# Optimization experiments

Hardware: AMD Instinct MI355X
Metric: run time of the kernel (lower is better)

## Reference

```python
import jax, jax.numpy as jnp
import numpy as np

B, S, D = 2, 2048, 1024
H, HD, K = 16, 64, 4
F = 4096
EPS = 1e-6
ROPE_BASE = 10000.0
NEG = -1e9


def rmsnorm(x, w):
    return x * jax.lax.rsqrt(jnp.mean(x * x, axis=-1, keepdims=True) + EPS) * w


def rope(t, pos):
    # t: (B,S,H,HD), pos: (B,S,H) per-node position (float)
    inv_freq = 1.0 / (ROPE_BASE ** (jnp.arange(0, HD, 2, dtype=jnp.float32) / HD))
    ang = pos[..., None] * inv_freq  # (B,S,H,HD/2)
    cos, sin = jnp.cos(ang), jnp.sin(ang)
    t1, t2 = t[..., : HD // 2], t[..., HD // 2:]
    return jnp.concatenate([t1 * cos - t2 * sin, t2 * cos + t1 * sin], axis=-1)


def setup_inputs() -> dict:
    key = jax.random.key(0)
    ks = jax.random.split(key, 12)
    s = lambda d: 1.0 / np.sqrt(d)
    return {
        "x": jax.random.normal(ks[0], (B, S, D), jnp.float32),
        "attn_norm_w": jnp.ones((D,), jnp.float32),
        "ffn_norm_w": jnp.ones((D,), jnp.float32),
        "Wq": jax.random.normal(ks[1], (D, H * HD), jnp.float32) * s(D),
        "Wk": jax.random.normal(ks[2], (D, H * HD), jnp.float32) * s(D),
        "Wv": jax.random.normal(ks[3], (D, H * HD), jnp.float32) * s(D),
        "Wo": jax.random.normal(ks[4], (H * HD, D), jnp.float32) * s(H * HD),
        "Wr": jax.random.normal(ks[5], (D, H * K), jnp.float32) * s(D),
        "w1": jax.random.normal(ks[6], (D, F), jnp.float32) * s(D),
        "w2": jax.random.normal(ks[7], (D, F), jnp.float32) * s(D),
        "w3": jax.random.normal(ks[8], (F, D), jnp.float32) * s(F),
    }


def reference(x, attn_norm_w, ffn_norm_w, Wq, Wk, Wv, Wo, Wr, w1, w2, w3):
    # ---- pre-norm + hypergraph node-routed causal attention ----
    h = rmsnorm(x, attn_norm_w)
    # per-(token, head) routing to K hyper-nodes
    logits = (h @ Wr).reshape(B, S, H, K)
    node = jnp.argmax(logits, axis=-1)                      # (B,S,H) int
    onehot = jax.nn.one_hot(node, K, dtype=jnp.float32)     # (B,S,H,K)
    # per-node RoPE position: count of previous same-node tokens
    cum = jnp.cumsum(onehot, axis=1)                        # inclusive
    pos = jnp.take_along_axis(cum, node[..., None], axis=-1)[..., 0] - 1.0  # (B,S,H)

    q = (h @ Wq).reshape(B, S, H, HD)
    k = (h @ Wk).reshape(B, S, H, HD)
    v = (h @ Wv).reshape(B, S, H, HD)
    q = rope(q, pos)
    k = rope(k, pos)

    scores = jnp.einsum("bqhd,bkhd->bhqk", q, k) / np.sqrt(HD)  # (B,H,S,S)
    node_h = jnp.transpose(node, (0, 2, 1))                     # (B,H,S)
    same = node_h[:, :, :, None] == node_h[:, :, None, :]       # intra-node only
    causal = jnp.tril(jnp.ones((S, S), bool))
    allowed = same & causal
    attn = jax.nn.softmax(jnp.where(allowed, scores, NEG), axis=-1)
    ctx = jnp.einsum("bhqk,bkhd->bqhd", attn, v).reshape(B, S, H * HD)
    x = x + ctx @ Wo

    # ---- pre-norm + SwiGLU ----
    h2 = rmsnorm(x, ffn_norm_w)
    ffn = (jax.nn.silu(h2 @ w1) * (h2 @ w2)) @ w3
    return x + ffn
```

## Files before the change

### kernel.cpp

```cpp
#include <hip/hip_runtime.h>
#include <hip/hip_bf16.h>
#include <math.h>

typedef __hip_bfloat16 bf16;

#define B_  2
#define S_  2048
#define D_  1024
#define H_  16
#define HD_ 64
#define KR_ 4
#define F_  4096
#define TOK (B_*S_)
#define NEG (-1.0e9f)

typedef __attribute__((ext_vector_type(8))) short bf16x8_t;
typedef __attribute__((ext_vector_type(4))) float f32x4_t;
typedef unsigned int u32;
#define AS1 __attribute__((address_space(1)))
#define AS3 __attribute__((address_space(3)))

__device__ __forceinline__ float u2f(unsigned short u) {
  union { float f; unsigned int i; } cv; cv.i = ((unsigned int)u) << 16; return cv.f;
}
__device__ __forceinline__ unsigned short f2u(float f) {
  return (unsigned short)(__bfloat16_as_ushort(__float2bfloat16(f)));
}

__device__ __forceinline__ void gl_lds16(const bf16* g, unsigned short* lds_base) {
  __builtin_amdgcn_global_load_lds((const AS1 u32*)g, (AS3 u32*)lds_base, 16, 0, 0);
}

__device__ __forceinline__ float rd1(const void* p, size_t i, bool isbf) {
  return isbf ? __bfloat162float(((const bf16*)p)[i]) : ((const float*)p)[i];
}

__device__ __forceinline__ void xcd_tile(int& bx, int& by) {
  const int nx = gridDim.x;
  const int nwg = nx * gridDim.y;
  const int hw = blockIdx.y * nx + blockIdx.x;
  const int tile = (hw & 7) * (nwg >> 3) + (hw >> 3);
  bx = tile % nx;
  by = tile / nx;
}

#define SWZ_SK8(lane)   (((((lane) & 3) ^ (((lane) >> 3) & 3))) << 3)
#define SWZ_RK(colv)    ((((colv) >> 1) & 3))

__global__ __launch_bounds__(256) void prep_k(
    const void* Wq, const void* Wk, const void* Wv, const void* Wo,
    const void* w1, const void* w2, const void* w3,
    bf16* __restrict__ qkvT, bf16* __restrict__ WoT,
    bf16* __restrict__ w1T, bf16* __restrict__ w2T, bf16* __restrict__ w3T,
    const void* Wr, float* __restrict__ Wrf,
    const unsigned* __restrict__ anw_words, int* __restrict__ flag) {
  const bool isbf = (anw_words[0] == 0x3F803F80u);
  const int bid = blockIdx.x;
  const int tid = threadIdx.x;
  if (bid == 0 && tid == 0) *flag = isbf ? 1 : 0;
  if (bid >= 16384) {
    const int i = (bid - 16384) * 256 + tid;
    Wrf[i] = rd1(Wr, i, isbf);
    return;
  }
  const void* W; bf16* WT; int K, N, nx, local;
  if (bid < 4096) {
    const int wi = bid >> 10; local = bid & 1023; K = 1024; N = 1024; nx = 32;
    W = (wi == 0) ? Wq : (wi == 1) ? Wk : (wi == 2) ? Wv : Wo;
    WT = (wi == 3) ? WoT : qkvT + ((size_t)wi << 20);
  } else if (bid < 8192)  { W = w1; WT = w1T; local = bid - 4096;  K = 1024; N = 4096; nx = 128; }
  else if (bid < 12288)   { W = w2; WT = w2T; local = bid - 8192;  K = 1024; N = 4096; nx = 128; }
  else                    { W = w3; WT = w3T; local = bid - 12288; K = 4096; N = 1024; nx = 32; }
  __shared__ float tile[32][33];
  const int n0 = (local % nx) * 32, k0 = (local / nx) * 32;
  const int rl = tid >> 5, cl = tid & 31;
#pragma unroll
  for (int i = 0; i < 4; i++)
    tile[rl + 8 * i][cl] = rd1(W, (size_t)(k0 + rl + 8 * i) * N + n0 + cl, isbf);
  __syncthreads();
#pragma unroll
  for (int i = 0; i < 4; i++)
    WT[(size_t)(n0 + rl + 8 * i) * K + k0 + cl] = __float2bfloat16(tile[cl][rl + 8 * i]);
}

template <bool XDUAL, bool WF>
__global__ __launch_bounds__(256) void rmsnorm_k(const void* x, const void* w,
                                                 bf16* __restrict__ ob,
                                                 float* __restrict__ of,
                                                 const int* __restrict__ flagp) {
  const bool isbf = (*flagp != 0);
  const int row = blockIdx.x;
  const int t = threadIdx.x;
  float v[4];
  float ss = 0.f;
#pragma unroll
  for (int i = 0; i < 4; i++) {
    const size_t idx = (size_t)row * D_ + t + 256 * i;
    v[i] = XDUAL ? rd1(x, idx, isbf) : ((const float*)x)[idx];
    ss += v[i] * v[i];
  }
#pragma unroll
  for (int off = 32; off >= 1; off >>= 1) ss += __shfl_down(ss, off);
  __shared__ float red[4];
  if ((t & 63) == 0) red[t >> 6] = ss;
  __syncthreads();
  const float tot = red[0] + red[1] + red[2] + red[3];
  const float sc = rsqrtf(tot * (1.f / D_) + 1e-6f);
#pragma unroll
  for (int i = 0; i < 4; i++) {
    const int c = t + 256 * i;
    const float r = v[i] * sc * rd1(w, c, isbf);
    ob[(size_t)row * D_ + c] = __float2bfloat16(r);
    if (WF) of[(size_t)row * D_ + c] = r;
  }
}

__global__ __launch_bounds__(256) void router_k(const float* __restrict__ h,
                                                const float* __restrict__ Wrf,
                                                int* __restrict__ node) {
  const int tok0 = blockIdx.x * 16;
  const int t = threadIdx.x;
  __shared__ float hs[16][1024];
  __shared__ float lg[16][64];
  {
    const float4* hsrc = (const float4*)(h + (size_t)tok0 * D_);
    float4* hdst = (float4*)hs;
#pragma unroll
    for (int j = 0; j < 16; j++) hdst[j * 256 + t] = hsrc[j * 256 + t];
  }
  __syncthreads();
  const int col = t & 63, tg = t >> 6;
  float acc[4] = {0.f, 0.f, 0.f, 0.f};
  for (int i = 0; i < D_; i += 4) {
    float wv[4];
#pragma unroll
    for (int u = 0; u < 4; u++) wv[u] = Wrf[(size_t)(i + u) * 64 + col];
#pragma unroll
    for (int tt = 0; tt < 4; tt++) {
      const float4 hv = *(const float4*)&hs[tg * 4 + tt][i];
      acc[tt] = fmaf(hv.x, wv[0], acc[tt]);
      acc[tt] = fmaf(hv.y, wv[1], acc[tt]);
      acc[tt] = fmaf(hv.z, wv[2], acc[tt]);
      acc[tt] = fmaf(hv.w, wv[3], acc[tt]);
    }
  }
#pragma unroll
  for (int tt = 0; tt < 4; tt++) lg[tg * 4 + tt][col] = acc[tt];
  __syncthreads();
  const int tok = t >> 4, hh = t & 15;
  const float* l = &lg[tok][hh * 4];
  float best = l[0];
  int bi = 0;
#pragma unroll
  for (int j = 1; j < KR_; j++) {
    const float vv = l[j];
    if (vv > best) { best = vv; bi = j; }
  }
  node[(size_t)(tok0 + tok) * H_ + hh] = bi;
}

__global__ __launch_bounds__(256) void pos_k(const int* __restrict__ node,
                                             float* __restrict__ pos,
                                             unsigned short* __restrict__ iperm,
                                             unsigned char* __restrict__ gid,
                                             int* __restrict__ gstart) {
  const int bh = blockIdx.x;
  const int b = bh >> 4, h = bh & 15;
  const int t = threadIdx.x;
  __shared__ int sc[256][4];
  int vals[8];
  int c[4] = {0, 0, 0, 0};
#pragma unroll
  for (int i = 0; i < 8; i++) {
    vals[i] = node[(size_t)(b * S_ + t * 8 + i) * H_ + h] & 3;
    c[vals[i]]++;
  }
#pragma unroll
  for (int n = 0; n < 4; n++) sc[t][n] = c[n];
  __syncthreads();
  for (int off = 1; off < 256; off <<= 1) {
    int add[4] = {0, 0, 0, 0};
    if (t >= off) {
#pragma unroll
      for (int n = 0; n < 4; n++) add[n] = sc[t - off][n];
    }
    __syncthreads();
#pragma unroll
    for (int n = 0; n < 4; n++) sc[t][n] += add[n];
    __syncthreads();
  }
  int start[4];
#pragma unroll
  for (int n = 0; n < 4; n++) start[n] = sc[t][n] - c[n];
  int gs[4];
  gs[0] = 0;
  gs[1] = sc[255][0];
  gs[2] = gs[1] + sc[255][1];
  gs[3] = gs[2] + sc[255][2];
  if (t < 4) gstart[bh * 4 + t] = gs[t];
  const size_t bhS = (size_t)bh * S_;
#pragma unroll
  for (int i = 0; i < 8; i++) {
    const int n = vals[i];
    const int rank = start[n]++;
    pos[(size_t)(b * S_ + t * 8 + i) * H_ + h] = (float)rank;
    const int newp = gs[n] + rank;
    iperm[bhS + newp] = (unsigned short)(t * 8 + i);
    gid[bhS + newp] = (unsigned char)n;
  }
}

__global__ __launch_bounds__(256) void attn_k(const bf16* __restrict__ q,
                                              const bf16* __restrict__ k,
                                              const bf16* __restrict__ v,
                                              const unsigned short* __restrict__ ip,
                                              const unsigned char* __restrict__ gidp,
                                              const int* __restrict__ gstart,
                                              bf16* __restrict__ ctx) {
  const int qt = 31 - blockIdx.x;
  const int h = blockIdx.y;
  const int b = blockIdx.z;
  const int bS = b * S_;
  const int bh = b * H_ + h;
  const size_t bhS = (size_t)bh * S_;
  const int tid = threadIdx.x;
  const int w = tid >> 6;
  const int lane = tid & 63;
  const int col = lane & 15;
  const int quad = lane >> 4;

  __shared__ unsigned short Qs[64][76];
  __shared__ unsigned short Ks[64][76];
  __shared__ unsigned short Vst[64][76];
  __shared__ unsigned short Pa[64][76];

  {
    const int qr = tid & 63, ds = (tid >> 6) * 16;
    const int ipq = ip[bhS + qt * 64 + qr];
    const bf16* src = q + (size_t)(bS + ipq) * D_ + h * HD_ + ds;
#pragma unroll
    for (int i = 0; i < 4; i++)
      *(ushort4*)&Qs[qr][ds + 4 * i] = *(const ushort4*)(src + 4 * i);
  }
  int gq_r[4];
#pragma unroll
  for (int reg = 0; reg < 4; reg++)
    gq_r[reg] = gidp[bhS + qt * 64 + w * 16 + quad * 4 + reg];
  float m_r[4] = {NEG, NEG, NEG, NEG};
  float l_r[4] = {0.f, 0.f, 0.f, 0.f};

  f32x4_t acc_o[4];
#pragma unroll
  for (int ct = 0; ct < 4; ct++) acc_o[ct] = (f32x4_t){0.f, 0.f, 0.f, 0.f};

  const int kt0 = gstart[bh * 4 + gidp[bhS + qt * 64]] >> 6;

  for (int kt = kt0; kt <= qt; kt++) {
    __syncthreads();
    {
      const int key = tid & 63, ds = (tid >> 6) * 16;
      const int ipk = ip[bhS + kt * 64 + key];
      const bf16* ksrc = k + (size_t)(bS + ipk) * D_ + h * HD_ + ds;
      const bf16* vsrc = v + (size_t)(bS + ipk) * D_ + h * HD_ + ds;
#pragma unroll
      for (int i = 0; i < 4; i++) {
        *(ushort4*)&Ks[key][ds + 4 * i] = *(const ushort4*)(ksrc + 4 * i);
        const ushort4 vu = *(const ushort4*)(vsrc + 4 * i);
        Vst[ds + 4 * i + 0][key] = vu.x;
        Vst[ds + 4 * i + 1][key] = vu.y;
        Vst[ds + 4 * i + 2][key] = vu.z;
        Vst[ds + 4 * i + 3][key] = vu.w;
      }
    }
    __syncthreads();

    f32x4_t s[4];
    {
      const bf16x8_t a0 = *(const bf16x8_t*)&Qs[w * 16 + col][quad * 8];
      const bf16x8_t a1 = *(const bf16x8_t*)&Qs[w * 16 + col][32 + quad * 8];
#pragma unroll
      for (int ct = 0; ct < 4; ct++) {
        f32x4_t acc = (f32x4_t){0.f, 0.f, 0.f, 0.f};
        const bf16x8_t b0 = *(const bf16x8_t*)&Ks[ct * 16 + col][quad * 8];
        const bf16x8_t b1 = *(const bf16x8_t*)&Ks[ct * 16 + col][32 + quad * 8];
        acc = __builtin_amdgcn_mfma_f32_16x16x32_bf16(a0, b0, acc, 0, 0, 0);
        acc = __builtin_amdgcn_mfma_f32_16x16x32_bf16(a1, b1, acc, 0, 0, 0);
        s[ct] = acc;
      }
    }
    const bool diag = (kt == qt);
    const size_t kbase = bhS + kt * 64;
    const int gk[4] = {gidp[kbase + col], gidp[kbase + 16 + col],
                       gidp[kbase + 32 + col], gidp[kbase + 48 + col]};
#pragma unroll
    for (int ct = 0; ct < 4; ct++) {
#pragma unroll
      for (int reg = 0; reg < 4; reg++) {
        const int qr = quad * 4 + reg;
        const int kc = ct * 16 + col;
        const bool ok = (gk[ct] == gq_r[reg]) && (!diag || kc <= w * 16 + qr);
        s[ct][reg] = ok ? (s[ct][reg] * 0.125f) : NEG;
      }
    }
    float al[4];
#pragma unroll
    for (int reg = 0; reg < 4; reg++) {
      float tm = fmaxf(fmaxf(s[0][reg], s[1][reg]), fmaxf(s[2][reg], s[3][reg]));
#pragma unroll
      for (int off = 1; off <= 8; off <<= 1) tm = fmaxf(tm, __shfl_xor(tm, off));
      const float mold = m_r[reg];
      const float mnew = fmaxf(mold, tm);
      const bool dead = (mnew <= -5.0e8f);
      const float alpha = dead ? 1.f : __expf(mold - mnew);
      float rowsum = 0.f;
      const int qr = w * 16 + quad * 4 + reg;
#pragma unroll
      for (int ct = 0; ct < 4; ct++) {
        const float e = dead ? 0.f : __expf(s[ct][reg] - mnew);
        rowsum += e;
        Pa[qr][ct * 16 + col] = f2u(e);
      }
#pragma unroll
      for (int off = 1; off <= 8; off <<= 1) rowsum += __shfl_xor(rowsum, off);
      l_r[reg] = l_r[reg] * alpha + rowsum;
      m_r[reg] = mnew;
      al[reg] = alpha;
    }
    {
      const bf16x8_t pa0 = *(const bf16x8_t*)&Pa[w * 16 + col][quad * 8];
      const bf16x8_t pa1 = *(const bf16x8_t*)&Pa[w * 16 + col][32 + quad * 8];
#pragma unroll
      for (int ct = 0; ct < 4; ct++) {
#pragma unroll
        for (int reg = 0; reg < 4; reg++) acc_o[ct][reg] *= al[reg];
        const bf16x8_t b0 = *(const bf16x8_t*)&Vst[ct * 16 + col][quad * 8];
        const bf16x8_t b1 = *(const bf16x8_t*)&Vst[ct * 16 + col][32 + quad * 8];
        acc_o[ct] = __builtin_amdgcn_mfma_f32_16x16x32_bf16(pa0, b0, acc_o[ct], 0, 0, 0);
        acc_o[ct] = __builtin_amdgcn_mfma_f32_16x16x32_bf16(pa1, b1, acc_o[ct], 0, 0, 0);
      }
    }
  }

#pragma unroll
  for (int reg = 0; reg < 4; reg++) {
    const int qr = w * 16 + quad * 4 + reg;
    const int op = ip[bhS + qt * 64 + qr];
    const float l = l_r[reg];
    const float invl = (l > 0.f) ? (1.f / l) : 0.f;
#pragma unroll
    for (int ct = 0; ct < 4; ct++) {
      ctx[(size_t)(bS + op) * D_ + h * HD_ + ct * 16 + col] =
          __float2bfloat16(acc_o[ct][reg] * invl);
    }
  }
}

template <int EPI>
__global__ __launch_bounds__(256) void mgemm_k(const bf16* __restrict__ A,
                                               const bf16* __restrict__ BT,
                                               float* __restrict__ Cf,
                                               void* Cout,
                                               const void* resdual,
                                               const float* __restrict__ resf,
                                               const float* __restrict__ posp,
                                               const int* __restrict__ flagp,
                                               int N, int Kd) {
  const bool isbf = (*flagp != 0);
  __shared__ unsigned short As[2][128][32];
  __shared__ unsigned short Bs[2][128][32];
  const int tid = threadIdx.x;
  const int w = tid >> 6, lane = tid & 63;
  const int col = lane & 15, quad = lane >> 4;
  const int wm = w & 1, wn = w >> 1;
  int bx, by;
  xcd_tile(bx, by);
  const int row0 = by * 128, col0 = bx * 128;

  const int srow = lane >> 2, sk8 = SWZ_SK8(lane);
  const bf16* Ag0 = A + (size_t)(row0 + 16 * w + srow) * Kd + sk8;
  const bf16* Ag1 = A + (size_t)(row0 + 64 + 16 * w + srow) * Kd + sk8;
  const bf16* Bg0 = BT + (size_t)(col0 + 16 * w + srow) * Kd + sk8;
  const bf16* Bg1 = BT + (size_t)(col0 + 64 + 16 * w + srow) * Kd + sk8;
  const int rk = SWZ_RK(col);

  f32x4_t acc[4][4];
#pragma unroll
  for (int i = 0; i < 4; i++)
#pragma unroll
    for (int j = 0; j < 4; j++) acc[i][j] = (f32x4_t){0.f, 0.f, 0.f, 0.f};

  gl_lds16(Ag0, &As[0][16 * w][0]);
  gl_lds16(Ag1, &As[0][64 + 16 * w][0]);
  gl_lds16(Bg0, &Bs[0][16 * w][0]);
  gl_lds16(Bg1, &Bs[0][64 + 16 * w][0]);
  __syncthreads();

  int cur = 0;
  for (int kt = 0; kt < Kd; kt += 32) {
    const int nxt = cur ^ 1;
    if (kt + 32 < Kd) {
      gl_lds16(Ag0 + kt + 32, &As[nxt][16 * w][0]);
      gl_lds16(Ag1 + kt + 32, &As[nxt][64 + 16 * w][0]);
      gl_lds16(Bg0 + kt + 32, &Bs[nxt][16 * w][0]);
      gl_lds16(Bg1 + kt + 32, &Bs[nxt][64 + 16 * w][0]);
    }
    bf16x8_t af[4], bfr[4];
#pragma unroll
    for (int i = 0; i < 4; i++) {
      af[i] = *(const bf16x8_t*)&As[cur][wm * 64 + i * 16 + col][(quad ^ rk) * 8];
      bfr[i] = *(const bf16x8_t*)&Bs[cur][wn * 64 + i * 16 + col][(quad ^ rk) * 8];
    }
#pragma unroll
    for (int i = 0; i < 4; i++)
#pragma unroll
      for (int j = 0; j < 4; j++)
        acc[i][j] = __builtin_amdgcn_mfma_f32_16x16x32_bf16(af[i], bfr[j], acc[i][j], 0, 0, 0);
    __syncthreads();
    cur = nxt;
  }

  if (EPI == 0) {
    const int ng_base = col0 + wn * 64;
    const int sec = ng_base >> 10;
    bf16* outp = (bf16*)Cout + (size_t)sec * ((size_t)TOK * D_);
    if (sec < 2) {
      const int hh = (ng_base & 1023) >> 6;
      const float c0 = 13.287712379549449f / 32.f;
      const float inv0 = exp2f(-(float)col * c0);
      const float inv1 = exp2f(-(float)(col + 16) * c0);
#pragma unroll
      for (int i = 0; i < 4; i++) {
#pragma unroll
        for (int reg = 0; reg < 4; reg++) {
          const int m = row0 + wm * 64 + i * 16 + quad * 4 + reg;
          const float p = posp[m * H_ + hh];
          float sn0, cs0, sn1, cs1;
          sincosf(p * inv0, &sn0, &cs0);
          sincosf(p * inv1, &sn1, &cs1);
          const float a0 = acc[i][0][reg], b0 = acc[i][2][reg];
          const float a1 = acc[i][1][reg], b1 = acc[i][3][reg];
          bf16* rowp = outp + (size_t)m * D_ + hh * 64;
          rowp[col]      = __float2bfloat16(a0 * cs0 - b0 * sn0);
          rowp[col + 32] = __float2bfloat16(b0 * cs0 + a0 * sn0);
          rowp[col + 16] = __float2bfloat16(a1 * cs1 - b1 * sn1);
          rowp[col + 48] = __float2bfloat16(b1 * cs1 + a1 * sn1);
        }
      }
    } else {
#pragma unroll
      for (int i = 0; i < 4; i++)
#pragma unroll
        for (int j = 0; j < 4; j++)
#pragma unroll
          for (int reg = 0; reg < 4; reg++) {
            const int m = row0 + wm * 64 + i * 16 + quad * 4 + reg;
            const int ng = col0 + wn * 64 + j * 16 + col;
            outp[(size_t)m * D_ + (ng & 1023)] = __float2bfloat16(acc[i][j][reg]);
          }
    }
  } else {
#pragma unroll
    for (int i = 0; i < 4; i++) {
#pragma unroll
      for (int j = 0; j < 4; j++) {
#pragma unroll
        for (int reg = 0; reg < 4; reg++) {
          const int m = row0 + wm * 64 + i * 16 + quad * 4 + reg;
          const int nl = wn * 64 + j * 16 + col;
          const size_t idx = (size_t)m * N + col0 + nl;
          if (EPI == 1) {
            Cf[idx] = acc[i][j][reg] + rd1(resdual, idx, isbf);
          } else {
            const float r = acc[i][j][reg] + resf[idx];
            if (isbf) ((bf16*)Cout)[idx] = __float2bfloat16(r);
            else      ((float*)Cout)[idx] = r;
          }
        }
      }
    }
  }
}

template <int EPI>
__global__ __launch_bounds__(256) void mgemm64_k(const bf16* __restrict__ A,
                                                 const bf16* __restrict__ BT,
                                                 float* __restrict__ Cf,
                                                 void* Cout,
                                                 const void* resdual,
                                                 const float* __restrict__ resf,
                                                 const int* __restrict__ flagp,
                                                 int N, int Kd) {
  const bool isbf = (*flagp != 0);
  __shared__ unsigned short As[2][2][64][32];
  __shared__ unsigned short Bs[2][2][128][32];
  const int tid = threadIdx.x;
  const int w = tid >> 6, lane = tid & 63;
  const int col = lane & 15, quad = lane >> 4;
  int bx, by;
  xcd_tile(bx, by);
  const int row0 = by * 64, col0 = bx * 128;

  const int srow = lane >> 2, sk8 = SWZ_SK8(lane);
  const bf16* Ag  = A + (size_t)(row0 + 16 * w + srow) * Kd + sk8;
  const bf16* Bg0 = BT + (size_t)(col0 + 32 * w + srow) * Kd + sk8;
  const bf16* Bg1 = BT + (size_t)(col0 + 32 * w + 16 + srow) * Kd + sk8;
  const int rk = SWZ_RK(col);

  f32x4_t acc[4][2];
#pragma unroll
  for (int i = 0; i < 4; i++)
#pragma unroll
    for (int j = 0; j < 2; j++) acc[i][j] = (f32x4_t){0.f, 0.f, 0.f, 0.f};

  auto stage = [&](int buf, int kt) {
#pragma unroll
    for (int hh = 0; hh < 2; hh++) {
      gl_lds16(Ag + kt + 32 * hh, &As[buf][hh][16 * w][0]);
      gl_lds16(Bg0 + kt + 32 * hh, &Bs[buf][hh][32 * w][0]);
      gl_lds16(Bg1 + kt + 32 * hh, &Bs[buf][hh][32 * w + 16][0]);
    }
  };

  stage(0, 0);
  __syncthreads();

  int cur = 0;
  for (int kt = 0; kt < Kd; kt += 64) {
    const int nxt = cur ^ 1;
    if (kt + 64 < Kd) stage(nxt, kt + 64);
#pragma unroll
    for (int hh = 0; hh < 2; hh++) {
      bf16x8_t af[4], bfr[2];
#pragma unroll
      for (int i = 0; i < 4; i++)
        af[i] = *(const bf16x8_t*)&As[cur][hh][i * 16 + col][(quad ^ rk) * 8];
#pragma unroll
      for (int j = 0; j < 2; j++)
        bfr[j] = *(const bf16x8_t*)&Bs[cur][hh][w * 32 + j * 16 + col][(quad ^ rk) * 8];
#pragma unroll
      for (int i = 0; i < 4; i++)
#pragma unroll
        for (int j = 0; j < 2; j++)
          acc[i][j] = __builtin_amdgcn_mfma_f32_16x16x32_bf16(af[i], bfr[j], acc[i][j], 0, 0, 0);
    }
    __syncthreads();
    cur = nxt;
  }

#pragma unroll
  for (int i = 0; i < 4; i++) {
#pragma unroll
    for (int j = 0; j < 2; j++) {
#pragma unroll
      for (int reg = 0; reg < 4; reg++) {
        const int m = row0 + i * 16 + quad * 4 + reg;
        const int nl = w * 32 + j * 16 + col;
        const size_t idx = (size_t)m * N + col0 + nl;
        if (EPI == 1) {
          Cf[idx] = acc[i][j][reg] + rd1(resdual, idx, isbf);
        } else {
          const float r = acc[i][j][reg] + resf[idx];
          if (isbf) ((bf16*)Cout)[idx] = __float2bfloat16(r);
          else      ((float*)Cout)[idx] = r;
        }
      }
    }
  }
}

__global__ __launch_bounds__(256) void mgate_k(const bf16* __restrict__ A,
                                               const bf16* __restrict__ B1T,
                                               const bf16* __restrict__ B2T,
                                               bf16* __restrict__ G,
                                               int Kd) {
  __shared__ unsigned short As[2][128][32];
  __shared__ unsigned short Bs1[2][64][32];
  __shared__ unsigned short Bs2[2][64][32];
  const int tid = threadIdx.x;
  const int w = tid >> 6, lane = tid & 63;
  const int col = lane & 15, quad = lane >> 4;
  const int wm = w & 1, wn = w >> 1;
  const int hw = blockIdx.y * gridDim.x + blockIdx.x;
  const int rect = hw & 7, inner = hw >> 3;
  const int by = ((rect >> 2) << 4) | (inner >> 4);
  const int bx = ((rect & 3) << 4) | (inner & 15);
  const int row0 = by * 128, col0 = bx * 64;

  const int srow = lane >> 2, sk8 = SWZ_SK8(lane);
  const bf16* Ag0 = A + (size_t)(row0 + 16 * w + srow) * Kd + sk8;
  const bf16* Ag1 = A + (size_t)(row0 + 64 + 16 * w + srow) * Kd + sk8;
  const bf16* B1g = B1T + (size_t)(col0 + 16 * w + srow) * Kd + sk8;
  const bf16* B2g = B2T + (size_t)(col0 + 16 * w + srow) * Kd + sk8;
  const int rk = SWZ_RK(col);

  f32x4_t acc1[4][2], acc2[4][2];
#pragma unroll
  for (int i = 0; i < 4; i++)
#pragma unroll
    for (int j = 0; j < 2; j++) {
      acc1[i][j] = (f32x4_t){0.f, 0.f, 0.f, 0.f};
      acc2[i][j] = (f32x4_t){0.f, 0.f, 0.f, 0.f};
    }

  gl_lds16(Ag0, &As[0][16 * w][0]);
  gl_lds16(Ag1, &As[0][64 + 16 * w][0]);
  gl_lds16(B1g, &Bs1[0][16 * w][0]);
  gl_lds16(B2g, &Bs2[0][16 * w][0]);
  __syncthreads();

  int cur = 0;
  for (int kt = 0; kt < Kd; kt += 32) {
    const int nxt = cur ^ 1;
    if (kt + 32 < Kd) {
      gl_lds16(Ag0 + kt + 32, &As[nxt][16 * w][0]);
      gl_lds16(Ag1 + kt + 32, &As[nxt][64 + 16 * w][0]);
      gl_lds16(B1g + kt + 32, &Bs1[nxt][16 * w][0]);
      gl_lds16(B2g + kt + 32, &Bs2[nxt][16 * w][0]);
    }
    bf16x8_t af[4], b1f[2], b2f[2];
#pragma unroll
    for (int i = 0; i < 4; i++)
      af[i] = *(const bf16x8_t*)&As[cur][wm * 64 + i * 16 + col][(quad ^ rk) * 8];
#pragma unroll
    for (int j = 0; j < 2; j++) {
      b1f[j] = *(const bf16x8_t*)&Bs1[cur][wn * 32 + j * 16 + col][(quad ^ rk) * 8];
      b2f[j] = *(const bf16x8_t*)&Bs2[cur][wn * 32 + j * 16 + col][(quad ^ rk) * 8];
    }
#pragma unroll
    for (int i = 0; i < 4; i++)
#pragma unroll
      for (int j = 0; j < 2; j++) {
        acc1[i][j] = __builtin_amdgcn_mfma_f32_16x16x32_bf16(af[i], b1f[j], acc1[i][j], 0, 0, 0);
        acc2[i][j] = __builtin_amdgcn_mfma_f32_16x16x32_bf16(af[i], b2f[j], acc2[i][j], 0, 0, 0);
      }
    __syncthreads();
    cur = nxt;
  }

#pragma unroll
  for (int i = 0; i < 4; i++) {
#pragma unroll
    for (int j = 0; j < 2; j++) {
#pragma unroll
      for (int reg = 0; reg < 4; reg++) {
        const int m = row0 + wm * 64 + i * 16 + quad * 4 + reg;
        const int n = col0 + wn * 32 + j * 16 + col;
        const float z = acc1[i][j][reg];
        const float sig = 1.f / (1.f + __expf(-z));
        G[(size_t)m * F_ + n] = __float2bfloat16(z * sig * acc2[i][j][reg]);
      }
    }
  }
}

extern "C" void kernel_launch(void* const* d_in, const int* in_sizes, int n_in,
                              void* d_out, int out_size, void* d_ws, size_t ws_size,
                              hipStream_t stream) {
  const void* x   = d_in[0];
  const void* anw = d_in[1];
  const void* fnw = d_in[2];
  const void* Wq  = d_in[3];
  const void* Wk  = d_in[4];
  const void* Wv  = d_in[5];
  const void* Wo  = d_in[6];
  const void* Wr  = d_in[7];
  const void* w1  = d_in[8];
  const void* w2  = d_in[9];
  const void* w3  = d_in[10];

  char* ws = (char*)d_ws;
  int*   node = (int*)ws;
  float* pos  = (float*)(ws + (256 << 10));
  int*   flag = (int*)(ws + (512 << 10));
  unsigned short* iperm = (unsigned short*)(ws + (640u << 10));
  unsigned char*  gidb  = (unsigned char*)(ws + (768u << 10));
  int*   gstart = (int*)(ws + (832u << 10));
  float* x2   = (float*)(ws + (1u << 20));
  bf16*  ctx  = (bf16*)(ws + (17u << 20));
  bf16*  h2   = ctx;
  float* Wrf  = (float*)(ws + (17u << 20));
  char*  r0   = ws + (25u << 20);
  bf16*  hb   = (bf16*)(r0);
  bf16*  qb   = (bf16*)(r0 + (8u << 20));
  bf16*  kb   = (bf16*)(r0 + (16u << 20));
  bf16*  vb   = (bf16*)(r0 + (24u << 20));
  float* hf   = (float*)(r0 + (8u << 20));
  bf16*  g    = (bf16*)(r0);
  bf16*  qkvT = (bf16*)(ws + (57u << 20));
  bf16*  WoT  = (bf16*)(ws + (63u << 20));
  bf16*  w1T  = (bf16*)(ws + (65u << 20));
  bf16*  w2T  = (bf16*)(ws + (73u << 20));
  bf16*  w3T  = (bf16*)(ws + (81u << 20));

  prep_k<<<16640, 256, 0, stream>>>(Wq, Wk, Wv, Wo, w1, w2, w3,
                                    qkvT, WoT, w1T, w2T, w3T,
                                    Wr, Wrf, (const unsigned*)anw, flag);
  rmsnorm_k<true, true><<<TOK, 256, 0, stream>>>(x, anw, hb, hf, flag);
  router_k<<<TOK / 16, 256, 0, stream>>>(hf, Wrf, node);
  pos_k<<<32, 256, 0, stream>>>(node, pos, iperm, gidb, gstart);
  mgemm_k<0><<<dim3(3072 / 128, TOK / 128), 256, 0, stream>>>(hb, qkvT, nullptr, qb, nullptr, nullptr, pos, flag, 3072, D_);
  attn_k<<<dim3(S_ / 64, H_, B_), 256, 0, stream>>>(qb, kb, vb, iperm, gidb, gstart, ctx);
  mgemm64_k<1><<<dim3(D_ / 128, TOK / 64), 256, 0, stream>>>(ctx, WoT, x2, nullptr, x, nullptr, flag, D_, D_);
  rmsnorm_k<false, false><<<TOK, 256, 0, stream>>>(x2, fnw, h2, nullptr, flag);
  mgate_k<<<dim3(F_ / 64, TOK / 128), 256, 0, stream>>>(h2, w1T, w2T, g, D_);
  mgemm64_k<2><<<dim3(D_ / 128, TOK / 64), 256, 0, stream>>>(g, w3T, nullptr, d_out, nullptr, x2, flag, D_, F_);
}
```

Baseline: 465.1 us.

## Triple-buffer LDS in GEMM kernels with partial vmcnt waits

Converts the three MFMA GEMM kernels from double-buffered to triple-buffered LDS staging with a prefetch distance of two k-tiles. __syncthreads is replaced by an explicit s_waitcnt vmcnt(n) plus s_barrier, so one tile's loads stay in flight while the current tile is consumed. mgemm64_k also moves from a 64-wide k step to a 32-wide one. This aims to hide global-to-LDS latency, at the cost of more LDS per block (possibly lower occupancy) and hand-counted waitcnt values that must match the number of outstanding loads.

New measurement: 473.8 us. No clear change (+1.9%).

```diff
diff --git a/kernel.cpp b/kernel.cpp
--- a/kernel.cpp
+++ b/kernel.cpp
@@ -46,6 +46,9 @@
 
 #define SWZ_SK8(lane)   (((((lane) & 3) ^ (((lane) >> 3) & 3))) << 3)
 #define SWZ_RK(colv)    ((((colv) >> 1) & 3))
+
+#define WAITCNT_BAR(n)  do { asm volatile("s_waitcnt vmcnt(" #n ")" ::: "memory"); \
+                             __builtin_amdgcn_s_barrier(); } while (0)
 
 __global__ __launch_bounds__(256) void prep_k(
     const void* Wq, const void* Wk, const void* Wv, const void* Wo,
@@ -366,8 +369,8 @@
                                                const int* __restrict__ flagp,
                                                int N, int Kd) {
   const bool isbf = (*flagp != 0);
-  __shared__ unsigned short As[2][128][32];
-  __shared__ unsigned short Bs[2][128][32];
+  __shared__ unsigned short As[3][128][32];
+  __shared__ unsigned short Bs[3][128][32];
   const int tid = threadIdx.x;
   const int w = tid >> 6, lane = tid & 63;
   const int col = lane & 15, quad = lane >> 4;
@@ -389,20 +392,23 @@
 #pragma unroll
     for (int j = 0; j < 4; j++) acc[i][j] = (f32x4_t){0.f, 0.f, 0.f, 0.f};
 
-  gl_lds16(Ag0, &As[0][16 * w][0]);
-  gl_lds16(Ag1, &As[0][64 + 16 * w][0]);
-  gl_lds16(Bg0, &Bs[0][16 * w][0]);
-  gl_lds16(Bg1, &Bs[0][64 + 16 * w][0]);
-  __syncthreads();
+  auto stage = [&](int buf, int kt) {
+    gl_lds16(Ag0 + kt, &As[buf][16 * w][0]);
+    gl_lds16(Ag1 + kt, &As[buf][64 + 16 * w][0]);
+    gl_lds16(Bg0 + kt, &Bs[buf][16 * w][0]);
+    gl_lds16(Bg1 + kt, &Bs[buf][64 + 16 * w][0]);
+  };
+
+  const int nt = Kd >> 5;
+  stage(0, 0);
+  stage(1, 32);
+  WAITCNT_BAR(4);
 
   int cur = 0;
-  for (int kt = 0; kt < Kd; kt += 32) {
-    const int nxt = cur ^ 1;
-    if (kt + 32 < Kd) {
-      gl_lds16(Ag0 + kt + 32, &As[nxt][16 * w][0]);
-      gl_lds16(Ag1 + kt + 32, &As[nxt][64 + 16 * w][0]);
-      gl_lds16(Bg0 + kt + 32, &Bs[nxt][16 * w][0]);
-      gl_lds16(Bg1 + kt + 32, &Bs[nxt][64 + 16 * w][0]);
+  for (int t = 0; t < nt; ++t) {
+    if (t + 2 < nt) {
+      const int pf = (cur + 2 >= 3) ? cur - 1 : cur + 2;
+      stage(pf, (t + 2) << 5);
     }
     bf16x8_t af[4], bfr[4];
 #pragma unroll
@@ -415,8 +421,11 @@
 #pragma unroll
       for (int j = 0; j < 4; j++)
         acc[i][j] = __builtin_amdgcn_mfma_f32_16x16x32_bf16(af[i], bfr[j], acc[i][j], 0, 0, 0);
-    __syncthreads();
-    cur = nxt;
+    if (t + 1 < nt) {
+      if (t + 2 < nt) WAITCNT_BAR(4);
+      else            WAITCNT_BAR(0);
+    }
+    cur = (cur + 1 >= 3) ? 0 : cur + 1;
   }
 
   if (EPI == 0) {
@@ -491,8 +500,8 @@
                                                  const int* __restrict__ flagp,
                                                  int N, int Kd) {
   const bool isbf = (*flagp != 0);
-  __shared__ unsigned short As[2][2][64][32];
-  __shared__ unsigned short Bs[2][2][128][32];
+  __shared__ unsigned short As[3][64][32];
+  __shared__ unsigned short Bs[3][128][32];
   const int tid = threadIdx.x;
   const int w = tid >> 6, lane = tid & 63;
   const int col = lane & 15, quad = lane >> 4;
@@ -513,38 +522,39 @@
     for (int j = 0; j < 2; j++) acc[i][j] = (f32x4_t){0.f, 0.f, 0.f, 0.f};
 
   auto stage = [&](int buf, int kt) {
-#pragma unroll
-    for (int hh = 0; hh < 2; hh++) {
-      gl_lds16(Ag + kt + 32 * hh, &As[buf][hh][16 * w][0]);
-      gl_lds16(Bg0 + kt + 32 * hh, &Bs[buf][hh][32 * w][0]);
-      gl_lds16(Bg1 + kt + 32 * hh, &Bs[buf][hh][32 * w + 16][0]);
-    }
+    gl_lds16(Ag + kt, &As[buf][16 * w][0]);
+    gl_lds16(Bg0 + kt, &Bs[buf][32 * w][0]);
+    gl_lds16(Bg1 + kt, &Bs[buf][32 * w + 16][0]);
   };
 
+  const int nt = Kd >> 5;
   stage(0, 0);
-  __syncthreads();
+  stage(1, 32);
+  WAITCNT_BAR(3);
 
   int cur = 0;
-  for (int kt = 0; kt < Kd; kt += 64) {
-    const int nxt = cur ^ 1;
-    if (kt + 64 < Kd) stage(nxt, kt + 64);
-#pragma unroll
-    for (int hh = 0; hh < 2; hh++) {
-      bf16x8_t af[4], bfr[2];
-#pragma unroll
-      for (int i = 0; i < 4; i++)
-        af[i] = *(const bf16x8_t*)&As[cur][hh][i * 16 + col][(quad ^ rk) * 8];
+  for (int t = 0; t < nt; ++t) {
+    if (t + 2 < nt) {
+      const int pf = (cur + 2 >= 3) ? cur - 1 : cur + 2;
+      stage(pf, (t + 2) << 5);
+    }
+    bf16x8_t af[4], bfr[2];
+#pragma unroll
+    for (int i = 0; i < 4; i++)
+      af[i] = *(const bf16x8_t*)&As[cur][i * 16 + col][(quad ^ rk) * 8];
+#pragma unroll
+    for (int j = 0; j < 2; j++)
+      bfr[j] = *(const bf16x8_t*)&Bs[cur][w * 32 + j * 16 + col][(quad ^ rk) * 8];
+#pragma unroll
+    for (int i = 0; i < 4; i++)
 #pragma unroll
       for (int j = 0; j < 2; j++)
-        bfr[j] = *(const bf16x8_t*)&Bs[cur][hh][w * 32 + j * 16 + col][(quad ^ rk) * 8];
-#pragma unroll
-      for (int i = 0; i < 4; i++)
-#pragma unroll
-        for (int j = 0; j < 2; j++)
-          acc[i][j] = __builtin_amdgcn_mfma_f32_16x16x32_bf16(af[i], bfr[j], acc[i][j], 0, 0, 0);
-    }
-    __syncthreads();
-    cur = nxt;
+        acc[i][j] = __builtin_amdgcn_mfma_f32_16x16x32_bf16(af[i], bfr[j], acc[i][j], 0, 0, 0);
+    if (t + 1 < nt) {
+      if (t + 2 < nt) WAITCNT_BAR(3);
+      else            WAITCNT_BAR(0);
+    }
+    cur = (cur + 1 >= 3) ? 0 : cur + 1;
   }
 
 #pragma unroll
@@ -573,9 +583,9 @@
                                                const bf16* __restrict__ B2T,
                                                bf16* __restrict__ G,
                                                int Kd) {
-  __shared__ unsigned short As[2][128][32];
-  __shared__ unsigned short Bs1[2][64][32];
-  __shared__ unsigned short Bs2[2][64][32];
+  __shared__ unsigned short As[3][128][32];
+  __shared__ unsigned short Bs1[3][64][32];
+  __shared__ unsigned short Bs2[3][64][32];
   const int tid = threadIdx.x;
   const int w = tid >> 6, lane = tid & 63;
   const int col = lane & 15, quad = lane >> 4;
@@ -602,20 +612,23 @@
       acc2[i][j] = (f32x4_t){0.f, 0.f, 0.f, 0.f};
     }
 
-  gl_lds16(Ag0, &As[0][16 * w][0]);
-  gl_lds16(Ag1, &As[0][64 + 16 * w][0]);
-  gl_lds16(B1g, &Bs1[0][16 * w][0]);
-  gl_lds16(B2g, &Bs2[0][16 * w][0]);
-  __syncthreads();
+  auto stage = [&](int buf, int kt) {
+    gl_lds16(Ag0 + kt, &As[buf][16 * w][0]);
+    gl_lds16(Ag1 + kt, &As[buf][64 + 16 * w][0]);
+    gl_lds16(B1g + kt, &Bs1[buf][16 * w][0]);
+    gl_lds16(B2g + kt, &Bs2[buf][16 * w][0]);
+  };
+
+  const int nt = Kd >> 5;
+  stage(0, 0);
+  stage(1, 32);
+  WAITCNT_BAR(4);
 
   int cur = 0;
-  for (int kt = 0; kt < Kd; kt += 32) {
-    const int nxt = cur ^ 1;
-    if (kt + 32 < Kd) {
-      gl_lds16(Ag0 + kt + 32, &As[nxt][16 * w][0]);
-      gl_lds16(Ag1 + kt + 32, &As[nxt][64 + 16 * w][0]);
-      gl_lds16(B1g + kt + 32, &Bs1[nxt][16 * w][0]);
-      gl_lds16(B2g + kt + 32, &Bs2[nxt][16 * w][0]);
+  for (int t = 0; t < nt; ++t) {
+    if (t + 2 < nt) {
+      const int pf = (cur + 2 >= 3) ? cur - 1 : cur + 2;
+      stage(pf, (t + 2) << 5);
     }
     bf16x8_t af[4], b1f[2], b2f[2];
 #pragma unroll
@@ -633,8 +646,11 @@
         acc1[i][j] = __builtin_amdgcn_mfma_f32_16x16x32_bf16(af[i], b1f[j], acc1[i][j], 0, 0, 0);
         acc2[i][j] = __builtin_amdgcn_mfma_f32_16x16x32_bf16(af[i], b2f[j], acc2[i][j], 0, 0, 0);
       }
-    __syncthreads();
-    cur = nxt;
+    if (t + 1 < nt) {
+      if (t + 2 < nt) WAITCNT_BAR(4);
+      else            WAITCNT_BAR(0);
+    }
+    cur = (cur + 1 >= 3) ? 0 : cur + 1;
   }
 
 #pragma unroll
```
